# Performance work log

Measured on AMD Instinct MI355X. Metric: run time of the kernel, lower is better.

Reference implementation:

```python
import jax, jax.numpy as jnp
import numpy as np

N = 100000   # nodes
E = 800000   # edges
H = 256      # hidden_dim == input_dim
L = 3        # num_layers
G = 64       # graphs in batch


def setup_inputs() -> dict:
    key = jax.random.key(0)
    ks = jax.random.split(key, 16)
    s = 0.05
    inp = {
        'x': jax.random.normal(ks[0], (N, H), jnp.float32),
        'edge_index': jax.random.randint(ks[1], (2, E), 0, N, dtype=jnp.int32),
        'batch': jnp.sort(jax.random.randint(ks[2], (N,), 0, G, dtype=jnp.int32)),
        'Ws': jax.random.normal(ks[3], (L, H, H), jnp.float32) * s,
        'Wn': jax.random.normal(ks[4], (L, H, H), jnp.float32) * s,
        'bs': jnp.zeros((L, H), jnp.float32),
        'att_w': jax.random.normal(ks[5], (H, 1), jnp.float32) * s,
        'att_b': jnp.zeros((1,), jnp.float32),
        'ne_W1': jax.random.normal(ks[6], (H, H // 2), jnp.float32) * s,
        'ne_b1': jnp.zeros((H // 2,), jnp.float32),
        'ne_W2': jax.random.normal(ks[7], (H // 2, 1), jnp.float32) * s,
        'ne_b2': jnp.zeros((1,), jnp.float32),
        'nd_W1': jax.random.normal(ks[8], (H, H // 2), jnp.float32) * s,
        'nd_b1': jnp.zeros((H // 2,), jnp.float32),
        'nd_W2': jax.random.normal(ks[9], (H // 2, 1), jnp.float32) * s,
        'nd_b2': jnp.zeros((1,), jnp.float32),
    }
    return inp


def reference(x, edge_index, batch, Ws, Wn, bs, att_w, att_b,
              ne_W1, ne_b1, ne_W2, ne_b2, nd_W1, nd_b1, nd_W2, nd_b2):
    src, dst = edge_index[0], edge_index[1]
    n = x.shape[0]
    # in-degree for mean aggregation (clamped to avoid div-by-zero)
    deg = jax.ops.segment_sum(jnp.ones(src.shape[0], x.dtype), dst, num_segments=n)
    deg = jnp.maximum(deg, 1.0)[:, None]                    # [N,1]
    # GNN encoder: SAGE-mean layers, ReLU (dropout identity at eval)
    h = x
    for l in range(Ws.shape[0]):
        msg = jax.ops.segment_sum(h[src], dst, num_segments=n) / deg  # [N,H]
        h = jax.nn.relu(h @ Ws[l] + msg @ Wn[l] + bs[l])
    # attention pooling: per-graph softmax over node scores
    s = (h @ att_w + att_b)[:, 0]                           # [N]
    m = jax.ops.segment_max(s, batch, num_segments=G)
    e = jnp.exp(s - m[batch])
    denom = jax.ops.segment_sum(e, batch, num_segments=G)
    alpha = (e / denom[batch])[:, None]                     # [N,1]
    g = jax.ops.segment_sum(alpha * h, batch, num_segments=G)  # [G,H]
    # heads: Linear-ReLU-(Dropout)-Linear
    graph_logits = jax.nn.relu(g @ ne_W1 + ne_b1) @ ne_W2 + ne_b2  # [G,1]
    node_logits = jax.nn.relu(h @ nd_W1 + nd_b1) @ nd_W2 + nd_b2  # [N,1]
    return (graph_logits, node_logits)
```

## Files before the change

kernel.cpp:

```cpp
#include <hip/hip_runtime.h>
#include <hip/hip_bf16.h>

#define HID 256
#define HHALF 128

typedef unsigned short u16;
typedef __attribute__((ext_vector_type(8))) short bf16x8;
typedef __attribute__((ext_vector_type(4))) float f32x4;

__device__ __forceinline__ float bf2f(unsigned int u) {
    unsigned int x = (u & 0xffffu) << 16;
    union { unsigned int i; float f; } c; c.i = x; return c.f;
}
__device__ __forceinline__ float lof(unsigned u) {
    union { unsigned i; float f; } c; c.i = u << 16; return c.f;
}
__device__ __forceinline__ float hif(unsigned u) {
    union { unsigned i; float f; } c; c.i = u & 0xffff0000u; return c.f;
}
__device__ __forceinline__ u16 f2bf(float f) {
    __hip_bfloat16 h = __float2bfloat16(f);
    union { __hip_bfloat16 h; u16 u; } c; c.h = h; return c.u;
}

__device__ __forceinline__ void gload16(const u16* g, u16* l) {
    __builtin_amdgcn_global_load_lds(
        (const __attribute__((address_space(1))) void*)g,
        (__attribute__((address_space(3))) void*)l, 16, 0, 0);
}

__global__ void k_count(const int* __restrict__ dst, int* __restrict__ cnt, int E) {
    int i = blockIdx.x * blockDim.x + threadIdx.x;
    if (i < E) atomicAdd(&cnt[dst[i]], 1);
}

__global__ void k_scan_block(const int* __restrict__ cnt, int* __restrict__ bsum, int n) {
    __shared__ int sd[256];
    int tid = threadIdx.x;
    int i = blockIdx.x * 256 + tid;
    int v = (i < n) ? cnt[i] : 0;
    sd[tid] = v; __syncthreads();
    for (int s = 128; s > 0; s >>= 1) {
        if (tid < s) sd[tid] += sd[tid + s];
        __syncthreads();
    }
    if (tid == 0) bsum[blockIdx.x] = sd[0];
}

__global__ void k_scan_top(int* __restrict__ bsum, int nb) {
    __shared__ int sd[512];
    int t = threadIdx.x;
    int v = (t < nb) ? bsum[t] : 0;
    sd[t] = v; __syncthreads();
    for (int s = 1; s < 512; s <<= 1) {
        int x = (t >= s) ? sd[t - s] : 0;
        __syncthreads();
        sd[t] += x;
        __syncthreads();
    }
    if (t < nb) bsum[t] = sd[t] - v;
}

__global__ void k_scan_down(const int* __restrict__ cnt, const int* __restrict__ boff,
                            int* __restrict__ row_off, int n, int total) {
    __shared__ int sd[256];
    int tid = threadIdx.x;
    int i = blockIdx.x * 256 + tid;
    int v = (i < n) ? cnt[i] : 0;
    sd[tid] = v; __syncthreads();
    for (int s = 1; s < 256; s <<= 1) {
        int x = (tid >= s) ? sd[tid - s] : 0;
        __syncthreads();
        sd[tid] += x;
        __syncthreads();
    }
    if (i < n) row_off[i] = boff[blockIdx.x] + sd[tid] - v;
    if (i == 0) row_off[n] = total;
}

__global__ void k_scatter(const int* __restrict__ src, const int* __restrict__ dst,
                          const int* __restrict__ row_off, int* __restrict__ fill,
                          int* __restrict__ col, int E) {
    int i = blockIdx.x * blockDim.x + threadIdx.x;
    if (i < E) {
        int d = dst[i];
        int p = atomicAdd(&fill[d], 1);
        col[row_off[d] + p] = src[i];
    }
}

__global__ void k_f2b(const float* __restrict__ in, u16* __restrict__ o, int total4) {
    int i = blockIdx.x * blockDim.x + threadIdx.x;
    if (i >= total4) return;
    float4 v = *(const float4*)&in[(size_t)i * 4];
    uint2 p;
    p.x = (unsigned)f2bf(v.x) | ((unsigned)f2bf(v.y) << 16);
    p.y = (unsigned)f2bf(v.z) | ((unsigned)f2bf(v.w) << 16);
    *(uint2*)&o[(size_t)i * 4] = p;
}

__global__ void k_wt_all(const float* __restrict__ Ws, const float* __restrict__ Wn,
                         const float* __restrict__ ndW1,
                         u16* __restrict__ WsT, u16* __restrict__ WnT,
                         u16* __restrict__ ndW1T, int L) {
    int idx = blockIdx.x * 256 + threadIdx.x;
    int mat = idx >> 16;
    int r = idx & 65535;
    int k = r >> 8, c = r & 255;
    if (mat < L) {
        WsT[(size_t)mat * 65536 + c * 256 + k] = f2bf(Ws[(size_t)mat * 65536 + k * 256 + c]);
    } else if (mat < 2 * L) {
        int l = mat - L;
        WnT[(size_t)l * 65536 + c * 256 + k] = f2bf(Wn[(size_t)l * 65536 + k * 256 + c]);
    } else {
        if (c < HHALF) ndW1T[c * 256 + k] = f2bf(ndW1[k * HHALF + c]);
    }
}

__global__ __launch_bounds__(256) void k_agg(
    const u16* __restrict__ h, const int* __restrict__ row_off,
    const int* __restrict__ col, u16* __restrict__ msg, int n) {
    int node = blockIdx.x * 4 + (threadIdx.x >> 6);
    if (node >= n) return;
    int lane = threadIdx.x & 63;
    int half = lane >> 5;
    int t = lane & 31;
    int s0 = row_off[node], s1 = row_off[node + 1];
    float a0 = 0.f, a1 = 0.f, a2 = 0.f, a3 = 0.f;
    float a4 = 0.f, a5 = 0.f, a6 = 0.f, a7 = 0.f;
    int e = s0;
    for (; e + 8 <= s1; e += 8) {
        int c0 = col[e + half];
        int c1 = col[e + 2 + half];
        int c2 = col[e + 4 + half];
        int c3 = col[e + 6 + half];
        uint4 v0 = *(const uint4*)&h[(size_t)c0 * HID + t * 8];
        uint4 v1 = *(const uint4*)&h[(size_t)c1 * HID + t * 8];
        uint4 v2 = *(const uint4*)&h[(size_t)c2 * HID + t * 8];
        uint4 v3 = *(const uint4*)&h[(size_t)c3 * HID + t * 8];
        a0 += (lof(v0.x) + lof(v1.x)) + (lof(v2.x) + lof(v3.x));
        a1 += (hif(v0.x) + hif(v1.x)) + (hif(v2.x) + hif(v3.x));
        a2 += (lof(v0.y) + lof(v1.y)) + (lof(v2.y) + lof(v3.y));
        a3 += (hif(v0.y) + hif(v1.y)) + (hif(v2.y) + hif(v3.y));
        a4 += (lof(v0.z) + lof(v1.z)) + (lof(v2.z) + lof(v3.z));
        a5 += (hif(v0.z) + hif(v1.z)) + (hif(v2.z) + hif(v3.z));
        a6 += (lof(v0.w) + lof(v1.w)) + (lof(v2.w) + lof(v3.w));
        a7 += (hif(v0.w) + hif(v1.w)) + (hif(v2.w) + hif(v3.w));
    }
    if (e < s1) {
        int i0 = e + half, i1 = e + 2 + half, i2 = e + 4 + half, i3 = e + 6 + half;
        float w0 = (i0 < s1) ? 1.f : 0.f; int c0 = col[(i0 < s1) ? i0 : s0];
        float w1 = (i1 < s1) ? 1.f : 0.f; int c1 = col[(i1 < s1) ? i1 : s0];
        float w2 = (i2 < s1) ? 1.f : 0.f; int c2 = col[(i2 < s1) ? i2 : s0];
        float w3 = (i3 < s1) ? 1.f : 0.f; int c3 = col[(i3 < s1) ? i3 : s0];
        uint4 v0 = *(const uint4*)&h[(size_t)c0 * HID + t * 8];
        uint4 v1 = *(const uint4*)&h[(size_t)c1 * HID + t * 8];
        uint4 v2 = *(const uint4*)&h[(size_t)c2 * HID + t * 8];
        uint4 v3 = *(const uint4*)&h[(size_t)c3 * HID + t * 8];
        a0 = fmaf(w0, lof(v0.x), fmaf(w1, lof(v1.x), fmaf(w2, lof(v2.x), fmaf(w3, lof(v3.x), a0))));
        a1 = fmaf(w0, hif(v0.x), fmaf(w1, hif(v1.x), fmaf(w2, hif(v2.x), fmaf(w3, hif(v3.x), a1))));
        a2 = fmaf(w0, lof(v0.y), fmaf(w1, lof(v1.y), fmaf(w2, lof(v2.y), fmaf(w3, lof(v3.y), a2))));
        a3 = fmaf(w0, hif(v0.y), fmaf(w1, hif(v1.y), fmaf(w2, hif(v2.y), fmaf(w3, hif(v3.y), a3))));
        a4 = fmaf(w0, lof(v0.z), fmaf(w1, lof(v1.z), fmaf(w2, lof(v2.z), fmaf(w3, lof(v3.z), a4))));
        a5 = fmaf(w0, hif(v0.z), fmaf(w1, hif(v1.z), fmaf(w2, hif(v2.z), fmaf(w3, hif(v3.z), a5))));
        a6 = fmaf(w0, lof(v0.w), fmaf(w1, lof(v1.w), fmaf(w2, lof(v2.w), fmaf(w3, lof(v3.w), a6))));
        a7 = fmaf(w0, hif(v0.w), fmaf(w1, hif(v1.w), fmaf(w2, hif(v2.w), fmaf(w3, hif(v3.w), a7))));
    }
    a0 += __shfl_xor(a0, 32); a1 += __shfl_xor(a1, 32);
    a2 += __shfl_xor(a2, 32); a3 += __shfl_xor(a3, 32);
    a4 += __shfl_xor(a4, 32); a5 += __shfl_xor(a5, 32);
    a6 += __shfl_xor(a6, 32); a7 += __shfl_xor(a7, 32);
    if (half == 0) {
        int deg = s1 - s0;
        float inv = 1.0f / (float)(deg > 1 ? deg : 1);
        uint4 o;
        o.x = (unsigned)f2bf(a0 * inv) | ((unsigned)f2bf(a1 * inv) << 16);
        o.y = (unsigned)f2bf(a2 * inv) | ((unsigned)f2bf(a3 * inv) << 16);
        o.z = (unsigned)f2bf(a4 * inv) | ((unsigned)f2bf(a5 * inv) << 16);
        o.w = (unsigned)f2bf(a6 * inv) | ((unsigned)f2bf(a7 * inv) << 16);
        *(uint4*)&msg[(size_t)node * HID + t * 8] = o;
    }
}

__global__ __launch_bounds__(512) void k_gemm_bf(
    const u16* __restrict__ A1, const u16* __restrict__ W1t,
    const u16* __restrict__ A2, const u16* __restrict__ W2t,
    const float* __restrict__ bias, u16* __restrict__ out,
    int n, int ncols,
    const float* __restrict__ dotw, const float* __restrict__ dotb,
    float* __restrict__ dotout) {
    __shared__ __align__(16) u16 As[128 * 64];
    __shared__ __align__(16) u16 Bs[256 * 64];
    const int tid  = threadIdx.x;
    const int lane = tid & 63;
    const int w    = tid >> 6;
    const int wr   = w >> 2, wc = w & 3;
    const int brow = blockIdx.x * 128;
    const int nkt  = A2 ? 8 : 4;

    f32x4 acc[4][4];
    #pragma unroll
    for (int m = 0; m < 4; ++m)
        #pragma unroll
        for (int q = 0; q < 4; ++q)
            acc[m][q] = (f32x4){0.f, 0.f, 0.f, 0.f};

    const int as0 = tid, as1 = tid + 512;
    int ar0 = brow + (as0 >> 3); if (ar0 >= n) ar0 = n - 1;
    int ar1 = brow + (as1 >> 3); if (ar1 >= n) ar1 = n - 1;
    const size_t asrc0 = (size_t)ar0 * HID + (size_t)(((as0 & 7) ^ (((as0 >> 3) >> 1) & 7)) * 8);
    const size_t asrc1 = (size_t)ar1 * HID + (size_t)(((as1 & 7) ^ (((as1 >> 3) >> 1) & 7)) * 8);
    u16* adst0 = &As[(w * 64) * 8];
    u16* adst1 = &As[(512 + w * 64) * 8];

    size_t bsrc[4];
    u16*   bdst[4];
    #pragma unroll
    for (int i = 0; i < 4; ++i) {
        int s = tid + i * 512;
        int row = s >> 3;
        bsrc[i] = (size_t)row * HID + (size_t)(((s & 7) ^ ((row >> 1) & 7)) * 8);
        bdst[i] = &Bs[(i * 512 + w * 64) * 8];
    }

    const int lr = lane & 15;
    const int lq = lane >> 4;
    const int swz = (lr >> 1) & 7;

    for (int kt = 0; kt < nkt; ++kt) {
        const u16* A = (kt < 4) ? A1 : A2;
        const u16* W = (kt < 4) ? W1t : W2t;
        const int k0 = (kt & 3) * 64;
        __syncthreads();
        gload16(A + asrc0 + k0, adst0);
        gload16(A + asrc1 + k0, adst1);
        gload16(W + bsrc[0] + k0, bdst[0]);
        gload16(W + bsrc[1] + k0, bdst[1]);
        gload16(W + bsrc[2] + k0, bdst[2]);
        gload16(W + bsrc[3] + k0, bdst[3]);
        __syncthreads();
        #pragma unroll
        for (int ks = 0; ks < 2; ++ks) {
            const int ch = (ks * 4 + lq) ^ swz;
            bf16x8 af[4], bg[4];
            #pragma unroll
            for (int m = 0; m < 4; ++m)
                af[m] = *(const bf16x8*)&As[(wr * 64 + m * 16 + lr) * 64 + ch * 8];
            #pragma unroll
            for (int q = 0; q < 4; ++q)
                bg[q] = *(const bf16x8*)&Bs[(wc * 64 + q * 16 + lr) * 64 + ch * 8];
            #pragma unroll
            for (int m = 0; m < 4; ++m)
                #pragma unroll
                for (int q = 0; q < 4; ++q)
                    acc[m][q] = __builtin_amdgcn_mfma_f32_16x16x32_bf16(
                        bg[q], af[m], acc[m][q], 0, 0, 0);
        }
    }

    #pragma unroll
    for (int m = 0; m < 4; ++m) {
        int row = brow + wr * 64 + m * 16 + lr;
        if (row >= n) continue;
        float dpart = 0.f;
        #pragma unroll
        for (int q = 0; q < 4; ++q) {
            int col = wc * 64 + q * 16 + lq * 4;
            if (col < ncols) {
                float4 bb = *(const float4*)&bias[col];
                float r0 = fmaxf(acc[m][q][0] + bb.x, 0.f);
                float r1 = fmaxf(acc[m][q][1] + bb.y, 0.f);
                float r2 = fmaxf(acc[m][q][2] + bb.z, 0.f);
                float r3 = fmaxf(acc[m][q][3] + bb.w, 0.f);
                if (out) {
                    uint2 o;
                    o.x = (unsigned)f2bf(r0) | ((unsigned)f2bf(r1) << 16);
                    o.y = (unsigned)f2bf(r2) | ((unsigned)f2bf(r3) << 16);
                    *(uint2*)&out[(size_t)row * ncols + col] = o;
                }
                if (dotout) {
                    float4 wv = *(const float4*)&dotw[col];
                    dpart += r0 * wv.x + r1 * wv.y + r2 * wv.z + r3 * wv.w;
                }
            }
        }
        if (dotout && (wc * 64 < ncols)) {
            dpart += __shfl_xor(dpart, 16);
            dpart += __shfl_xor(dpart, 32);
            if (lane < 16) {
                float add = dpart + ((wc == 0) ? dotb[0] : 0.f);
                atomicAdd(&dotout[row], add);
            }
        }
    }
}

__global__ __launch_bounds__(256) void k_ndhead(
    const u16* __restrict__ A1, const u16* __restrict__ W1t,
    const float* __restrict__ bias, int n,
    const float* __restrict__ dotw, const float* __restrict__ dotb,
    float* __restrict__ dotout) {
    __shared__ __align__(16) u16 As[128 * 64];
    __shared__ __align__(16) u16 Bs[128 * 64];
    const int tid  = threadIdx.x;
    const int lane = tid & 63;
    const int w    = tid >> 6;
    const int wr   = w >> 1, wc = w & 1;
    const int brow = blockIdx.x * 128;

    f32x4 acc[4][4];
    #pragma unroll
    for (int m = 0; m < 4; ++m)
        #pragma unroll
        for (int q = 0; q < 4; ++q)
            acc[m][q] = (f32x4){0.f, 0.f, 0.f, 0.f};

    size_t asrc[4], bsrc[4];
    u16 *adst[4], *bdst[4];
    #pragma unroll
    for (int i = 0; i < 4; ++i) {
        int s = tid + i * 256;
        int row = s >> 3;
        int ch = ((s & 7) ^ ((row >> 1) & 7)) * 8;
        int ar = brow + row; if (ar >= n) ar = n - 1;
        asrc[i] = (size_t)ar * HID + ch;
        bsrc[i] = (size_t)row * HID + ch;
        adst[i] = &As[(i * 256 + w * 64) * 8];
        bdst[i] = &Bs[(i * 256 + w * 64) * 8];
    }

    const int lr = lane & 15;
    const int lq = lane >> 4;
    const int swz = (lr >> 1) & 7;

    for (int kt = 0; kt < 4; ++kt) {
        const int k0 = kt * 64;
        __syncthreads();
        #pragma unroll
        for (int i = 0; i < 4; ++i) gload16(A1 + asrc[i] + k0, adst[i]);
        #pragma unroll
        for (int i = 0; i < 4; ++i) gload16(W1t + bsrc[i] + k0, bdst[i]);
        __syncthreads();
        #pragma unroll
        for (int ks = 0; ks < 2; ++ks) {
            const int ch = (ks * 4 + lq) ^ swz;
            bf16x8 af[4], bg[4];
            #pragma unroll
            for (int m = 0; m < 4; ++m)
                af[m] = *(const bf16x8*)&As[(wr * 64 + m * 16 + lr) * 64 + ch * 8];
            #pragma unroll
            for (int q = 0; q < 4; ++q)
                bg[q] = *(const bf16x8*)&Bs[(wc * 64 + q * 16 + lr) * 64 + ch * 8];
            #pragma unroll
            for (int m = 0; m < 4; ++m)
                #pragma unroll
                for (int q = 0; q < 4; ++q)
                    acc[m][q] = __builtin_amdgcn_mfma_f32_16x16x32_bf16(
                        bg[q], af[m], acc[m][q], 0, 0, 0);
        }
    }

    #pragma unroll
    for (int m = 0; m < 4; ++m) {
        int row = brow + wr * 64 + m * 16 + lr;
        if (row >= n) continue;
        float dpart = 0.f;
        #pragma unroll
        for (int q = 0; q < 4; ++q) {
            int col = wc * 64 + q * 16 + lq * 4;
            float4 bb = *(const float4*)&bias[col];
            float4 wv = *(const float4*)&dotw[col];
            dpart += fmaxf(acc[m][q][0] + bb.x, 0.f) * wv.x
                   + fmaxf(acc[m][q][1] + bb.y, 0.f) * wv.y
                   + fmaxf(acc[m][q][2] + bb.z, 0.f) * wv.z
                   + fmaxf(acc[m][q][3] + bb.w, 0.f) * wv.w;
        }
        dpart += __shfl_xor(dpart, 16);
        dpart += __shfl_xor(dpart, 32);
        if (lane < 16) {
            float add = dpart + ((wc == 0) ? dotb[0] : 0.f);
            atomicAdd(&dotout[row], add);
        }
    }
}

__global__ void k_gstart(const int* __restrict__ batch, int* __restrict__ gstart, int n, int G) {
    int i = blockIdx.x * blockDim.x + threadIdx.x;
    if (i >= n) return;
    int b = batch[i];
    int bp = (i == 0) ? -1 : batch[i - 1];
    for (int g = bp + 1; g <= b; ++g) gstart[g] = i;
    if (i == n - 1) {
        for (int g = b + 1; g <= G; ++g) gstart[g] = n;
    }
}

__global__ void k_mdenom(const float* __restrict__ s, const int* __restrict__ gstart,
                         float* __restrict__ m, float* __restrict__ denom) {
    int g = blockIdx.x;
    int t = threadIdx.x;
    int i0 = gstart[g], i1 = gstart[g + 1];
    __shared__ float red[256];
    float mx = -INFINITY;
    for (int i = i0 + t; i < i1; i += 256) mx = fmaxf(mx, s[i]);
    red[t] = mx; __syncthreads();
    for (int st = 128; st; st >>= 1) {
        if (t < st) red[t] = fmaxf(red[t], red[t + st]);
        __syncthreads();
    }
    float gm = red[0];
    __syncthreads();
    float sm = 0.f;
    for (int i = i0 + t; i < i1; i += 256) sm += expf(s[i] - gm);
    red[t] = sm; __syncthreads();
    for (int st = 128; st; st >>= 1) {
        if (t < st) red[t] += red[t + st];
        __syncthreads();
    }
    if (t == 0) { m[g] = gm; denom[g] = red[0]; }
}

__global__ void k_pool(const u16* __restrict__ h, const float* __restrict__ sarr,
                       const float* __restrict__ marr, const float* __restrict__ denom,
                       const int* __restrict__ gstart, float* __restrict__ gpool) {
    int g = blockIdx.x, sp = blockIdx.y, t = threadIdx.x;
    int i0 = gstart[g], i1 = gstart[g + 1];
    int len = i1 - i0;
    int a = i0 + (int)((long long)len * sp / 16);
    int b = i0 + (int)((long long)len * (sp + 1) / 16);
    float dn = denom[g];
    float inv = (dn > 0.f) ? 1.0f / dn : 0.f;
    float mg = marr[g];
    float acc = 0.f;
    for (int i = a; i < b; ++i)
        acc += expf(sarr[i] - mg) * inv * bf2f(h[(size_t)i * HID + t]);
    if (acc != 0.f || sp == 0) atomicAdd(&gpool[g * HID + t], acc);
}

__global__ void k_ghead(const float* __restrict__ gpool, const float* __restrict__ W1,
                        const float* __restrict__ b1, const float* __restrict__ W2,
                        const float* __restrict__ b2, float* __restrict__ out) {
    int g = blockIdx.x, t = threadIdx.x;
    __shared__ float row[HID];
    __shared__ float red[128];
    row[t] = gpool[g * HID + t];
    row[t + 128] = gpool[g * HID + t + 128];
    __syncthreads();
    float acc = 0.f;
    #pragma unroll 8
    for (int k = 0; k < HID; ++k) acc = fmaf(row[k], W1[k * HHALF + t], acc);
    float hid = fmaxf(acc + b1[t], 0.f);
    red[t] = hid * W2[t];
    __syncthreads();
    for (int st = 64; st; st >>= 1) {
        if (t < st) red[t] += red[t + st];
        __syncthreads();
    }
    if (t == 0) out[g] = red[0] + b2[0];
}

extern "C" void kernel_launch(void* const* d_in, const int* in_sizes, int n_in,
                              void* d_out, int out_size, void* d_ws, size_t ws_size,
                              hipStream_t stream) {
    const float* x      = (const float*)d_in[0];
    const int*   eidx   = (const int*)d_in[1];
    const int*   batch  = (const int*)d_in[2];
    const float* Ws     = (const float*)d_in[3];
    const float* Wn     = (const float*)d_in[4];
    const float* bs     = (const float*)d_in[5];
    const float* att_w  = (const float*)d_in[6];
    const float* att_b  = (const float*)d_in[7];
    const float* ne_W1  = (const float*)d_in[8];
    const float* ne_b1  = (const float*)d_in[9];
    const float* ne_W2  = (const float*)d_in[10];
    const float* ne_b2  = (const float*)d_in[11];
    const float* nd_W1  = (const float*)d_in[12];
    const float* nd_b1  = (const float*)d_in[13];
    const float* nd_W2  = (const float*)d_in[14];
    const float* nd_b2  = (const float*)d_in[15];
    float* out = (float*)d_out;

    const int N = in_sizes[2];
    const int E = in_sizes[1] / 2;
    const int L = in_sizes[3] / (HID * HID);
    const int G = out_size - N;

    const int* src = eidx;
    const int* dst = eidx + E;

    size_t off = 0;
    auto alloc = [&](size_t bytes) {
        void* p = (char*)d_ws + off;
        off += (bytes + 255) & ~(size_t)255;
        return p;
    };
    int*   cnt     = (int*)alloc((size_t)N * 4);
    int*   row_off = (int*)alloc((size_t)(N + 1) * 4);
    int*   fill    = (int*)alloc((size_t)N * 4);
    int*   col     = (int*)alloc((size_t)E * 4);
    int*   gstart  = (int*)alloc((size_t)(G + 1) * 4);
    int*   bsum    = (int*)alloc(1024 * 4);
    float* sarr    = (float*)alloc((size_t)N * 4);
    float* marr    = (float*)alloc((size_t)G * 4);
    float* denom   = (float*)alloc((size_t)G * 4);
    float* gpool   = (float*)alloc((size_t)G * HID * 4);
    u16*   xb      = (u16*)alloc((size_t)N * HID * 2);
    u16*   msgb    = (u16*)alloc((size_t)N * HID * 2);
    u16*   hb1     = (u16*)alloc((size_t)N * HID * 2);
    u16*   hb2     = (u16*)alloc((size_t)N * HID * 2);
    u16*   WsT     = (u16*)alloc((size_t)L * HID * HID * 2);
    u16*   WnT     = (u16*)alloc((size_t)L * HID * HID * 2);
    u16*   ndW1T   = (u16*)alloc((size_t)HID * HID * 2);
    (void)ws_size;

    const int eb = (E + 255) / 256;
    const int nb = (N + 255) / 256;

    hipMemsetAsync(cnt, 0, (size_t)N * 4, stream);
    k_count<<<eb, 256, 0, stream>>>(dst, cnt, E);
    k_scan_block<<<nb, 256, 0, stream>>>(cnt, bsum, N);
    k_scan_top<<<1, 512, 0, stream>>>(bsum, nb);
    k_scan_down<<<nb, 256, 0, stream>>>(cnt, bsum, row_off, N, E);
    hipMemsetAsync(fill, 0, (size_t)N * 4, stream);
    k_scatter<<<eb, 256, 0, stream>>>(src, dst, row_off, fill, col, E);

    k_f2b<<<(N * HID / 4 + 255) / 256, 256, 0, stream>>>(x, xb, N * HID / 4);
    k_wt_all<<<(2 * L + 1) * (HID * HID / 256), 256, 0, stream>>>(
        Ws, Wn, nd_W1, WsT, WnT, ndW1T, L);

    hipMemsetAsync(sarr, 0, (size_t)N * 4, stream);
    hipMemsetAsync(out + G, 0, (size_t)N * 4, stream);

    const int gx = (N + 127) / 128;
    const u16* hin = xb;
    u16* hout = hb1;
    for (int l = 0; l < L; ++l) {
        bool last = (l == L - 1);
        k_agg<<<(N + 3) / 4, 256, 0, stream>>>(hin, row_off, col, msgb, N);
        k_gemm_bf<<<gx, 512, 0, stream>>>(
            hin, WsT + (size_t)l * HID * HID, msgb, WnT + (size_t)l * HID * HID,
            bs + (size_t)l * HID, hout, N, HID,
            last ? att_w : nullptr, last ? att_b : nullptr, last ? sarr : nullptr);
        hin = hout;
        hout = (hout == hb1) ? hb2 : hb1;
    }
    const u16* h = hin;

    k_gstart<<<nb, 256, 0, stream>>>(batch, gstart, N, G);
    k_mdenom<<<G, 256, 0, stream>>>(sarr, gstart, marr, denom);
    hipMemsetAsync(gpool, 0, (size_t)G * HID * 4, stream);
    k_pool<<<dim3(G, 16), HID, 0, stream>>>(h, sarr, marr, denom, gstart, gpool);

    k_ghead<<<G, HHALF, 0, stream>>>(gpool, ne_W1, ne_b1, ne_W2, ne_b2, out);

    k_ndhead<<<gx, 256, 0, stream>>>(
        h, ndW1T, nd_b1, N, nd_W2, nd_b2, out + G);
}
```

Measured before the change: 536.1 us.

## Double-buffer LDS tiles in the bf16 GEMM with K-step of 32

Splits the GEMM K loop into 32-wide steps and keeps two LDS buffers for A and W, so the global-to-LDS load for the next step is issued before the MFMAs of the current step. This drops one barrier per iteration and is meant to hide global load latency behind matrix math. The cost is twice as many loop iterations with fewer MFMAs per barrier. The swizzle is redone for the narrower 4-chunk rows.

```diff
diff --git a/kernel.cpp b/kernel.cpp
--- a/kernel.cpp
+++ b/kernel.cpp
@@ -189,14 +189,14 @@
     int n, int ncols,
     const float* __restrict__ dotw, const float* __restrict__ dotb,
     float* __restrict__ dotout) {
-    __shared__ __align__(16) u16 As[128 * 64];
-    __shared__ __align__(16) u16 Bs[256 * 64];
+    __shared__ __align__(16) u16 As[2][128 * 32];
+    __shared__ __align__(16) u16 Bs[2][256 * 32];
     const int tid  = threadIdx.x;
     const int lane = tid & 63;
     const int w    = tid >> 6;
     const int wr   = w >> 2, wc = w & 3;
     const int brow = blockIdx.x * 128;
-    const int nkt  = A2 ? 8 : 4;
+    const int nkt  = A2 ? 16 : 8;
 
     f32x4 acc[4][4];
     #pragma unroll
@@ -205,57 +205,53 @@
         for (int q = 0; q < 4; ++q)
             acc[m][q] = (f32x4){0.f, 0.f, 0.f, 0.f};
 
-    const int as0 = tid, as1 = tid + 512;
-    int ar0 = brow + (as0 >> 3); if (ar0 >= n) ar0 = n - 1;
-    int ar1 = brow + (as1 >> 3); if (ar1 >= n) ar1 = n - 1;
-    const size_t asrc0 = (size_t)ar0 * HID + (size_t)(((as0 & 7) ^ (((as0 >> 3) >> 1) & 7)) * 8);
-    const size_t asrc1 = (size_t)ar1 * HID + (size_t)(((as1 & 7) ^ (((as1 >> 3) >> 1) & 7)) * 8);
-    u16* adst0 = &As[(w * 64) * 8];
-    u16* adst1 = &As[(512 + w * 64) * 8];
-
-    size_t bsrc[4];
-    u16*   bdst[4];
-    #pragma unroll
-    for (int i = 0; i < 4; ++i) {
-        int s = tid + i * 512;
-        int row = s >> 3;
-        bsrc[i] = (size_t)row * HID + (size_t)(((s & 7) ^ ((row >> 1) & 7)) * 8);
-        bdst[i] = &Bs[(i * 512 + w * 64) * 8];
-    }
+    const int arow_t = w * 16 + (lane >> 2);
+    int arow = brow + arow_t; if (arow >= n) arow = n - 1;
+    const int ach = (lane & 3) ^ ((arow_t >> 1) & 3);
+    const size_t abase = (size_t)arow * HID + ach * 8;
+    const int As_off = (w * 16) * 32;
+
+    const int brow0 = w * 32 + (lane >> 2);
+    const int bch0  = (lane & 3) ^ ((brow0 >> 1) & 3);
+    const size_t bbase0 = (size_t)brow0 * HID + bch0 * 8;
+    const int Bs_off0 = (w * 32) * 32;
+    const int brow1 = brow0 + 16;
+    const int bch1  = (lane & 3) ^ ((brow1 >> 1) & 3);
+    const size_t bbase1 = (size_t)brow1 * HID + bch1 * 8;
+    const int Bs_off1 = (w * 32 + 16) * 32;
 
     const int lr = lane & 15;
     const int lq = lane >> 4;
-    const int swz = (lr >> 1) & 7;
-
+    const int ph = lq ^ ((lr >> 1) & 3);
+
+    auto stage = [&](int t) {
+        const u16* A = (t < 8) ? A1 : A2;
+        const u16* W = (t < 8) ? W1t : W2t;
+        const int k0 = (t & 7) * 32;
+        const int b = t & 1;
+        gload16(A + abase + k0, &As[b][As_off]);
+        gload16(W + bbase0 + k0, &Bs[b][Bs_off0]);
+        gload16(W + bbase1 + k0, &Bs[b][Bs_off1]);
+    };
+
+    stage(0);
     for (int kt = 0; kt < nkt; ++kt) {
-        const u16* A = (kt < 4) ? A1 : A2;
-        const u16* W = (kt < 4) ? W1t : W2t;
-        const int k0 = (kt & 3) * 64;
-        __syncthreads();
-        gload16(A + asrc0 + k0, adst0);
-        gload16(A + asrc1 + k0, adst1);
-        gload16(W + bsrc[0] + k0, bdst[0]);
-        gload16(W + bsrc[1] + k0, bdst[1]);
-        gload16(W + bsrc[2] + k0, bdst[2]);
-        gload16(W + bsrc[3] + k0, bdst[3]);
-        __syncthreads();
-        #pragma unroll
-        for (int ks = 0; ks < 2; ++ks) {
-            const int ch = (ks * 4 + lq) ^ swz;
-            bf16x8 af[4], bg[4];
-            #pragma unroll
-            for (int m = 0; m < 4; ++m)
-                af[m] = *(const bf16x8*)&As[(wr * 64 + m * 16 + lr) * 64 + ch * 8];
+        __syncthreads();
+        if (kt + 1 < nkt) stage(kt + 1);
+        const int b = kt & 1;
+        bf16x8 af[4], bg[4];
+        #pragma unroll
+        for (int m = 0; m < 4; ++m)
+            af[m] = *(const bf16x8*)&As[b][(wr * 64 + m * 16 + lr) * 32 + ph * 8];
+        #pragma unroll
+        for (int q = 0; q < 4; ++q)
+            bg[q] = *(const bf16x8*)&Bs[b][(wc * 64 + q * 16 + lr) * 32 + ph * 8];
+        #pragma unroll
+        for (int m = 0; m < 4; ++m)
             #pragma unroll
             for (int q = 0; q < 4; ++q)
-                bg[q] = *(const bf16x8*)&Bs[(wc * 64 + q * 16 + lr) * 64 + ch * 8];
-            #pragma unroll
-            for (int m = 0; m < 4; ++m)
-                #pragma unroll
-                for (int q = 0; q < 4; ++q)
-                    acc[m][q] = __builtin_amdgcn_mfma_f32_16x16x32_bf16(
-                        bg[q], af[m], acc[m][q], 0, 0, 0);
-        }
+                acc[m][q] = __builtin_amdgcn_mfma_f32_16x16x32_bf16(
+                    bg[q], af[m], acc[m][q], 0, 0, 0);
     }
 
     #pragma unroll
```

New measurement: 612.9 us. 1.14x slower.
